# Kernel optimization log

Measured on AMD Instinct MI355X. Metric: run time of the kernel, lower is better.

Reference implementation:

```python
import jax, jax.numpy as jnp
import numpy as np

H = 16
D_MODEL = 1024
B, S = 2, 2048
DH = D_MODEL // H


def setup_inputs() -> dict:
    key = jax.random.key(0)
    ks = jax.random.split(key, 12)
    std = 0.02
    q = jax.random.normal(ks[0], (B, S, D_MODEL), dtype=jnp.float32)
    k = jax.random.normal(ks[1], (B, S, D_MODEL), dtype=jnp.float32)
    v = jax.random.normal(ks[2], (B, S, D_MODEL), dtype=jnp.float32)
    # additive causal mask: 0 on/below diagonal, -1e9 above
    causal = jnp.tril(jnp.ones((S, S), dtype=bool))
    mask = jnp.where(causal, 0.0, -1e9).astype(jnp.float32)[None, None, :, :]
    def dense(kk):
        return (jax.random.normal(kk, (D_MODEL, D_MODEL), dtype=jnp.float32) * std,
                jnp.zeros((D_MODEL,), dtype=jnp.float32))
    Wq, bq = dense(ks[3])
    Wk, bk = dense(ks[4])
    Wv, bv = dense(ks[5])
    Wo, bo = dense(ks[6])
    return {"q": q, "k": k, "v": v, "mask": mask,
            "Wq": Wq, "bq": bq, "Wk": Wk, "bk": bk,
            "Wv": Wv, "bv": bv, "Wo": Wo, "bo": bo}


def reference(q, k, v, mask, Wq, bq, Wk, bk, Wv, bv, Wo, bo):
    b, s, d = q.shape
    def split_heads(x):  # [b,s,d] -> [b,h,s,dh]
        return x.reshape(b, s, H, DH).transpose(0, 2, 1, 3)
    qh = split_heads(q @ Wq + bq)
    kh = split_heads(k @ Wk + bk)
    vh = split_heads(v @ Wv + bv)
    scale = 1.0 / jnp.sqrt(jnp.asarray(DH, dtype=qh.dtype))
    scores = jnp.einsum('bhqd,bhkd->bhqk', qh, kh) * scale + mask
    weights = jax.nn.softmax(scores, axis=-1)
    ctx = jnp.einsum('bhqk,bhkd->bhqd', weights, vh)
    ctx = ctx.transpose(0, 2, 1, 3).reshape(b, s, d)
    return ctx @ Wo + bo
```

## Files before the change

### kernel.cpp

```cpp
#include <hip/hip_runtime.h>
#include <hip/hip_bf16.h>
#include <stdint.h>

typedef __bf16 bf16x8 __attribute__((ext_vector_type(8)));
typedef float  f32x4  __attribute__((ext_vector_type(4)));
typedef __hip_bfloat16 bf16_t;

#define D_MODEL 1024
#define NH 16
#define DH 64
#define BB 2
#define SS 2048
#define MTOT (BB*SS)
#define NQT (SS/64)

#define GBM 128
#define GBN 64
#define GBK 64

__global__ void cvt_qkv_kernel(const float* __restrict__ q, const float* __restrict__ k,
                               const float* __restrict__ v, bf16_t* __restrict__ dst) {
  const int n1v = MTOT * D_MODEL / 4;
  int tid = blockIdx.x * blockDim.x + threadIdx.x;
  int stride = gridDim.x * blockDim.x;
  for (int i = tid; i < 3 * n1v; i += stride) {
    int which = i / n1v;
    int j = i - which * n1v;
    const float4* src = (const float4*)(which == 0 ? q : (which == 1 ? k : v));
    float4 f = src[j];
    union { bf16_t h[4]; short4 s4; } u;
    u.h[0] = __float2bfloat16(f.x);
    u.h[1] = __float2bfloat16(f.y);
    u.h[2] = __float2bfloat16(f.z);
    u.h[3] = __float2bfloat16(f.w);
    ((short4*)dst)[(size_t)which * n1v + j] = u.s4;
  }
}

__global__ void transpose_w_kernel(const float* __restrict__ W0, const float* __restrict__ W1,
                                   const float* __restrict__ W2, const float* __restrict__ W3,
                                   bf16_t* __restrict__ WtAll) {
  __shared__ float tile[32][33];
  const int z = blockIdx.z;
  const float* W = (z == 0) ? W0 : (z == 1) ? W1 : (z == 2) ? W2 : W3;
  bf16_t* Wt = WtAll + (size_t)z * D_MODEL * D_MODEL;
  const int tx = threadIdx.x, ty = threadIdx.y;
  const int bx = blockIdx.x, by = blockIdx.y;
#pragma unroll
  for (int i = 0; i < 4; ++i)
    tile[ty + i * 8][tx] = W[(size_t)(by * 32 + ty + i * 8) * D_MODEL + bx * 32 + tx];
  __syncthreads();
#pragma unroll
  for (int i = 0; i < 4; ++i)
    Wt[(size_t)(bx * 32 + ty + i * 8) * D_MODEL + by * 32 + tx] =
        __float2bfloat16(tile[tx][ty + i * 8]);
}

__device__ __forceinline__ void g2lds16(const bf16_t* g, bf16_t* l) {
  __builtin_amdgcn_global_load_lds((__attribute__((address_space(1))) void*)(g),
                                   (__attribute__((address_space(3))) void*)(l), 16, 0, 0);
}

__device__ __forceinline__ void gemm_tile_mainloop(const bf16_t* __restrict__ A,
                                                   const bf16_t* __restrict__ Bt,
                                                   bf16_t* As, bf16_t* Bs,
                                                   int m0, int n0, f32x4 acc[4][2]) {
  const int tid = threadIdx.x;
  const int wv = tid >> 6, ln = tid & 63;
  const int wr = wv >> 1, wc = wv & 1;
  const int lr = ln & 15, lg = ln >> 4;

#pragma unroll
  for (int mi = 0; mi < 4; ++mi)
#pragma unroll
    for (int ni = 0; ni < 2; ++ni)
      acc[mi][ni] = (f32x4){0.f, 0.f, 0.f, 0.f};

  for (int kt = 0; kt < D_MODEL / GBK; ++kt) {
#pragma unroll
    for (int c = 0; c < 6; ++c) {
      int chunk = wv * 6 + c;
      int row8 = ln >> 3;
      int col = (ln & 7) * 8;
      if (chunk < 16) {
        g2lds16(A  + (size_t)(m0 + chunk * 8 + row8) * D_MODEL + kt * GBK + col,
                As + chunk * 8 * GBK);
      } else {
        g2lds16(Bt + (size_t)(n0 + (chunk - 16) * 8 + row8) * D_MODEL + kt * GBK + col,
                Bs + (chunk - 16) * 8 * GBK);
      }
    }
    __syncthreads();
#pragma unroll
    for (int ks = 0; ks < 2; ++ks) {
      bf16x8 af[4], bfr[2];
#pragma unroll
      for (int mi = 0; mi < 4; ++mi)
        af[mi] = *(const bf16x8*)(As + (size_t)(wr * 64 + mi * 16 + lr) * GBK + ks * 32 + lg * 8);
#pragma unroll
      for (int ni = 0; ni < 2; ++ni)
        bfr[ni] = *(const bf16x8*)(Bs + (size_t)(wc * 32 + ni * 16 + lr) * GBK + ks * 32 + lg * 8);
#pragma unroll
      for (int mi = 0; mi < 4; ++mi)
#pragma unroll
        for (int ni = 0; ni < 2; ++ni)
          acc[mi][ni] = __builtin_amdgcn_mfma_f32_16x16x32_bf16(af[mi], bfr[ni], acc[mi][ni], 0, 0, 0);
    }
    __syncthreads();
  }
}

__global__ __launch_bounds__(256)
void proj_gemm_kernel(const bf16_t* __restrict__ Aq, const bf16_t* __restrict__ Ak,
                      const bf16_t* __restrict__ Av, const bf16_t* __restrict__ WtAll,
                      const float* __restrict__ bq, const float* __restrict__ bk,
                      const float* __restrict__ bv,
                      bf16_t* __restrict__ Qg, bf16_t* __restrict__ Kg,
                      bf16_t* __restrict__ Vt) {
  __shared__ bf16_t As[GBM * GBK];
  __shared__ bf16_t Bs[GBN * GBK];
  const int z = blockIdx.z;
  const bf16_t* A = (z == 0) ? Aq : (z == 1) ? Ak : Av;
  const bf16_t* Bt = WtAll + (size_t)z * D_MODEL * D_MODEL;
  const float* bias = (z == 0) ? bq : (z == 1) ? bk : bv;
  const int m0 = blockIdx.y * GBM, n0 = blockIdx.x * GBN;

  f32x4 acc[4][2];
  gemm_tile_mainloop(A, Bt, As, Bs, m0, n0, acc);

  const int tid = threadIdx.x;
  const int wv = tid >> 6, ln = tid & 63;
  const int wr = wv >> 1, wc = wv & 1;
  const int lr = ln & 15, lg = ln >> 4;

#pragma unroll
  for (int mi = 0; mi < 4; ++mi) {
#pragma unroll
    for (int ni = 0; ni < 2; ++ni) {
      int ncol = n0 + wc * 32 + ni * 16 + lr;
      float bsv = bias[ncol];
#pragma unroll
      for (int j = 0; j < 4; ++j) {
        int mrow = m0 + wr * 64 + mi * 16 + lg * 4 + j;
        bf16_t hv = __float2bfloat16(acc[mi][ni][j] + bsv);
        if (z == 0) {
          Qg[(size_t)mrow * D_MODEL + ncol] = hv;
        } else if (z == 1) {
          Kg[(size_t)mrow * D_MODEL + ncol] = hv;
        } else {
          int b = mrow >> 11, s = mrow & (SS - 1);
          Vt[(size_t)((b << 10) | ncol) * SS + s] = hv;
        }
      }
    }
  }
}

__global__ __launch_bounds__(256)
void out_gemm_kernel(const bf16_t* __restrict__ Ctx, const bf16_t* __restrict__ Wto,
                     const float* __restrict__ bo, float* __restrict__ out) {
  __shared__ bf16_t As[GBM * GBK];
  __shared__ bf16_t Bs[GBN * GBK];
  const int m0 = blockIdx.y * GBM, n0 = blockIdx.x * GBN;

  f32x4 acc[4][2];
  gemm_tile_mainloop(Ctx, Wto, As, Bs, m0, n0, acc);

  const int tid = threadIdx.x;
  const int wv = tid >> 6, ln = tid & 63;
  const int wr = wv >> 1, wc = wv & 1;
  const int lr = ln & 15, lg = ln >> 4;

#pragma unroll
  for (int mi = 0; mi < 4; ++mi) {
#pragma unroll
    for (int ni = 0; ni < 2; ++ni) {
      int ncol = n0 + wc * 32 + ni * 16 + lr;
      float bsv = bo[ncol];
#pragma unroll
      for (int j = 0; j < 4; ++j) {
        int mrow = m0 + wr * 64 + mi * 16 + lg * 4 + j;
        out[(size_t)mrow * D_MODEL + ncol] = acc[mi][ni][j] + bsv;
      }
    }
  }
}

__device__ __forceinline__ uint32_t pack2bf(float a, float b) {
  union { __hip_bfloat16 h; unsigned short u; } ua, ub;
  ua.h = __float2bfloat16(a);
  ub.h = __float2bfloat16(b);
  return (uint32_t)ua.u | ((uint32_t)ub.u << 16);
}

#define PSTRIDE 44

__device__ __forceinline__ void attn_run(
    f32x4 acc_o[2][4], f32x4 acc_l[2], float m_run[2],
    const bf16x8 qf[2][2], const bf16_t* Kbase, const bf16_t* Vbase,
    uint32_t (*P32)[PSTRIDE], int q0, int t0, int t1, int lr, int lg, bf16x8 onesf) {
  bf16x8 kf_cur[2][4];
#pragma unroll
  for (int ks = 0; ks < 2; ++ks)
#pragma unroll
    for (int kb = 0; kb < 4; ++kb)
      kf_cur[ks][kb] = *(const bf16x8*)(Kbase + (size_t)(t0 * 64 + kb * 16 + lr) * D_MODEL + ks * 32 + lg * 8);

  for (int t = t0; t < t1; ++t) {
    const int kv0 = t * 64;
    f32x4 sc[2][4];
#pragma unroll
    for (int qi = 0; qi < 2; ++qi)
#pragma unroll
      for (int kb = 0; kb < 4; ++kb) sc[qi][kb] = (f32x4){0.f, 0.f, 0.f, 0.f};

    __builtin_amdgcn_s_setprio(1);
#pragma unroll
    for (int ks = 0; ks < 2; ++ks) {
#pragma unroll
      for (int kb = 0; kb < 4; ++kb) {
        sc[0][kb] = __builtin_amdgcn_mfma_f32_16x16x32_bf16(kf_cur[ks][kb], qf[0][ks], sc[0][kb], 0, 0, 0);
        sc[1][kb] = __builtin_amdgcn_mfma_f32_16x16x32_bf16(kf_cur[ks][kb], qf[1][ks], sc[1][kb], 0, 0, 0);
      }
    }
    __builtin_amdgcn_s_setprio(0);

    bf16x8 kf_nxt[2][4];
    if (t + 1 < t1) {
#pragma unroll
      for (int ks = 0; ks < 2; ++ks)
#pragma unroll
        for (int kb = 0; kb < 4; ++kb)
          kf_nxt[ks][kb] = *(const bf16x8*)(Kbase + (size_t)(kv0 + 64 + kb * 16 + lr) * D_MODEL + ks * 32 + lg * 8);
    }
    bf16x8 vf[2][4];
#pragma unroll
    for (int ks = 0; ks < 2; ++ks)
#pragma unroll
      for (int db = 0; db < 4; ++db)
        vf[ks][db] = *(const bf16x8*)(Vbase + (size_t)(db * 16 + lr) * SS + kv0 + ks * 32 + lg * 8);

    if (kv0 + 63 > q0) {
#pragma unroll
      for (int qi = 0; qi < 2; ++qi) {
        int qc = q0 + qi * 16 + lr;
#pragma unroll
        for (int kb = 0; kb < 4; ++kb)
#pragma unroll
          for (int r = 0; r < 4; ++r) {
            int kc = kv0 + kb * 16 + 4 * lg + r;
            if (kc > qc) sc[qi][kb][r] = -1e30f;
          }
      }
    }

#pragma unroll
    for (int qi = 0; qi < 2; ++qi) {
      float vm = sc[qi][0][0];
#pragma unroll
      for (int kb = 0; kb < 4; ++kb)
#pragma unroll
        for (int r = 0; r < 4; ++r) vm = fmaxf(vm, sc[qi][kb][r]);
      vm = fmaxf(vm, __shfl_xor(vm, 16, 64));
      vm = fmaxf(vm, __shfl_xor(vm, 32, 64));
      float mo = m_run[qi];
      float mn = fmaxf(mo, vm);
      float scl = __expf(mo - mn);
      m_run[qi] = mn;
#pragma unroll
      for (int kb = 0; kb < 4; ++kb)
#pragma unroll
        for (int hh = 0; hh < 2; ++hh) {
          float p0 = __expf(sc[qi][kb][2 * hh]     - mn);
          float p1 = __expf(sc[qi][kb][2 * hh + 1] - mn);
          P32[qi * 16 + lr][8 * kb + 2 * lg + hh] = pack2bf(p0, p1);
        }
#pragma unroll
      for (int r = 0; r < 4; ++r) acc_l[qi][r] *= scl;
#pragma unroll
      for (int db = 0; db < 4; ++db)
#pragma unroll
        for (int r = 0; r < 4; ++r) acc_o[qi][db][r] *= scl;
    }

    asm volatile("s_waitcnt lgkmcnt(0)" ::: "memory");
    __builtin_amdgcn_sched_barrier(0);

    bf16x8 pb[2][2];
#pragma unroll
    for (int qi = 0; qi < 2; ++qi)
#pragma unroll
      for (int ks = 0; ks < 2; ++ks)
        pb[qi][ks] = *(const bf16x8*)&P32[qi * 16 + lr][16 * ks + 4 * lg];

    __builtin_amdgcn_s_setprio(1);
#pragma unroll
    for (int ks = 0; ks < 2; ++ks) {
#pragma unroll
      for (int qi = 0; qi < 2; ++qi) {
        acc_l[qi] = __builtin_amdgcn_mfma_f32_16x16x32_bf16(onesf, pb[qi][ks], acc_l[qi], 0, 0, 0);
#pragma unroll
        for (int db = 0; db < 4; ++db)
          acc_o[qi][db] = __builtin_amdgcn_mfma_f32_16x16x32_bf16(vf[ks][db], pb[qi][ks], acc_o[qi][db], 0, 0, 0);
      }
    }
    __builtin_amdgcn_s_setprio(0);

    if (t + 1 < t1) {
#pragma unroll
      for (int ks = 0; ks < 2; ++ks)
#pragma unroll
        for (int kb = 0; kb < 4; ++kb)
          kf_cur[ks][kb] = kf_nxt[ks][kb];
    }
  }
}

__device__ __forceinline__ void attn_load_q(bf16x8 qf[2][2], const bf16_t* Qbase,
                                            int q0, int lr, int lg) {
#pragma unroll
  for (int qi = 0; qi < 2; ++qi)
#pragma unroll
    for (int ks = 0; ks < 2; ++ks) {
      bf16x8 raw = *(const bf16x8*)(Qbase + (size_t)(q0 + qi * 16 + lr) * D_MODEL + ks * 32 + lg * 8);
#pragma unroll
      for (int j = 0; j < 8; ++j) raw[j] = (__bf16)((float)raw[j] * 0.125f);
      qf[qi][ks] = raw;
    }
}

__device__ __forceinline__ void attn_init(f32x4 acc_o[2][4], f32x4 acc_l[2], float m_run[2]) {
#pragma unroll
  for (int qi = 0; qi < 2; ++qi) {
#pragma unroll
    for (int db = 0; db < 4; ++db) acc_o[qi][db] = (f32x4){0.f, 0.f, 0.f, 0.f};
    acc_l[qi] = (f32x4){0.f, 0.f, 0.f, 0.f};
    m_run[qi] = -1e30f;
  }
}

__device__ __forceinline__ void store_ctx_tile(
    uint32_t (*P32)[PSTRIDE], const f32x4 acc_o[2][4], const f32x4 acc_l[2],
    bf16_t* __restrict__ Ctx, int b, int h, int q0, int ln, int lr, int lg) {
#pragma unroll
  for (int qi = 0; qi < 2; ++qi) {
    float rl = 1.0f / acc_l[qi][0];
#pragma unroll
    for (int db = 0; db < 4; ++db)
#pragma unroll
      for (int hh = 0; hh < 2; ++hh)
        P32[qi * 16 + lr][8 * db + 2 * lg + hh] =
            pack2bf(acc_o[qi][db][2 * hh] * rl, acc_o[qi][db][2 * hh + 1] * rl);
  }
  asm volatile("s_waitcnt lgkmcnt(0)" ::: "memory");
  __builtin_amdgcn_sched_barrier(0);
#pragma unroll
  for (int c = 0; c < 4; ++c) {
    int row = (ln >> 2) + 16 * (c >> 1);
    int dwc = (ln & 3) * 4 + 16 * (c & 1);
    bf16x8 v = *(const bf16x8*)&P32[row][dwc];
    *(bf16x8*)(Ctx + (size_t)(b * SS + q0 + row) * D_MODEL + h * DH + dwc * 2) = v;
  }
}

__global__ __launch_bounds__(256)
void attn_kernel(const bf16_t* __restrict__ Qg, const bf16_t* __restrict__ Kg,
                 const bf16_t* __restrict__ Vt, bf16_t* __restrict__ Ctx) {
  __shared__ __align__(16) uint32_t P32[4][32][PSTRIDE];
  __shared__ __align__(16) float O_part[2][32][68];
  __shared__ float ml_part[2][32][2];
  const int bh = blockIdx.x;
  const int pp = blockIdx.y;
  const int b = bh >> 4, h = bh & 15;
  const int wv = threadIdx.x >> 6, ln = threadIdx.x & 63;
  const int lr = ln & 15, lg = ln >> 4;

  const int qt_lo = pp, qt_hi = NQT - 1 - pp;
  const int h0 = 16 - pp;
  const int rh = wv & 1;

  const size_t qkbase = (size_t)b * SS * D_MODEL + (size_t)h * DH;
  const bf16_t* Qbase = Qg + qkbase;
  const bf16_t* Kbase = Kg + qkbase;
  const bf16_t* Vbase = Vt + (size_t)(bh * 64) * SS;

  bf16x8 onesf;
#pragma unroll
  for (int j = 0; j < 8; ++j) onesf[j] = (__bf16)1.0f;

  bf16x8 qf[2][2];
  f32x4 acc_o[2][4];
  f32x4 acc_l[2];
  float m_run[2];
  const int q0_hi = qt_hi * 64 + rh * 32;

  if (wv < 2) {
    const int q0_lo = qt_lo * 64 + rh * 32;
    attn_load_q(qf, Qbase, q0_lo, lr, lg);
    attn_init(acc_o, acc_l, m_run);
    attn_run(acc_o, acc_l, m_run, qf, Kbase, Vbase, P32[wv], q0_lo, 0, pp + 1, lr, lg, onesf);
    store_ctx_tile(P32[wv], acc_o, acc_l, Ctx, b, h, q0_lo, ln, lr, lg);

    attn_load_q(qf, Qbase, q0_hi, lr, lg);
    attn_init(acc_o, acc_l, m_run);
    attn_run(acc_o, acc_l, m_run, qf, Kbase, Vbase, P32[wv], q0_hi, 0, h0, lr, lg, onesf);
  } else {
    attn_load_q(qf, Qbase, q0_hi, lr, lg);
    attn_init(acc_o, acc_l, m_run);
    attn_run(acc_o, acc_l, m_run, qf, Kbase, Vbase, P32[wv], q0_hi, h0, NQT - pp, lr, lg, onesf);
    const int pidx = wv - 2;
#pragma unroll
    for (int qi = 0; qi < 2; ++qi) {
#pragma unroll
      for (int db = 0; db < 4; ++db)
        *(f32x4*)&O_part[pidx][qi * 16 + lr][16 * db + 4 * lg] = acc_o[qi][db];
      if (lg == 0) {
        ml_part[pidx][qi * 16 + lr][0] = m_run[qi];
        ml_part[pidx][qi * 16 + lr][1] = acc_l[qi][0];
      }
    }
  }

  __syncthreads();

  if (wv < 2) {
#pragma unroll
    for (int qi = 0; qi < 2; ++qi) {
      float m1 = m_run[qi];
      float m2 = ml_part[wv][qi * 16 + lr][0];
      float mn = fmaxf(m1, m2);
      float a1 = __expf(m1 - mn);
      float a2 = __expf(m2 - mn);
      float l = a1 * acc_l[qi][0] + a2 * ml_part[wv][qi * 16 + lr][1];
#pragma unroll
      for (int db = 0; db < 4; ++db) {
        f32x4 po = *(const f32x4*)&O_part[wv][qi * 16 + lr][16 * db + 4 * lg];
#pragma unroll
        for (int r = 0; r < 4; ++r)
          acc_o[qi][db][r] = a1 * acc_o[qi][db][r] + a2 * po[r];
      }
      acc_l[qi] = (f32x4){l, l, l, l};
    }
    store_ctx_tile(P32[wv], acc_o, acc_l, Ctx, b, h, q0_hi, ln, lr, lg);
  }
}

extern "C" void kernel_launch(void* const* d_in, const int* in_sizes, int n_in,
                              void* d_out, int out_size, void* d_ws, size_t ws_size,
                              hipStream_t stream) {
  const float* q  = (const float*)d_in[0];
  const float* k  = (const float*)d_in[1];
  const float* v  = (const float*)d_in[2];
  const float* bq = (const float*)d_in[5];
  const float* bk = (const float*)d_in[7];
  const float* bv = (const float*)d_in[9];
  const float* bo = (const float*)d_in[11];
  const float* Wq = (const float*)d_in[4];
  const float* Wk = (const float*)d_in[6];
  const float* Wv = (const float*)d_in[8];
  const float* Wo = (const float*)d_in[10];
  float* out = (float*)d_out;

  char* w = (char*)d_ws;
  bf16_t* Aqkv  = (bf16_t*)(w);
  bf16_t* WtAll = (bf16_t*)(w + 25165824);
  bf16_t* Qg    = (bf16_t*)(w + 33554432);
  bf16_t* Kg    = (bf16_t*)(w + 41943040);
  bf16_t* Vt    = (bf16_t*)(w + 50331648);
  bf16_t* Ctx   = (bf16_t*)(w + 58720256);

  cvt_qkv_kernel<<<2048, 256, 0, stream>>>(q, k, v, Aqkv);
  transpose_w_kernel<<<dim3(32, 32, 4), dim3(32, 8), 0, stream>>>(Wq, Wk, Wv, Wo, WtAll);
  proj_gemm_kernel<<<dim3(16, 32, 3), 256, 0, stream>>>(
      Aqkv, Aqkv + (size_t)MTOT * D_MODEL, Aqkv + 2 * (size_t)MTOT * D_MODEL,
      WtAll, bq, bk, bv, Qg, Kg, Vt);
  attn_kernel<<<dim3(32, 16), 256, 0, stream>>>(Qg, Kg, Vt, Ctx);
  out_gemm_kernel<<<dim3(16, 32), 256, 0, stream>>>(
      Ctx, WtAll + 3 * (size_t)D_MODEL * D_MODEL, bo, out);
}
```

Baseline: 275.6 us.

## Compute V-transpose projection directly as Wv^T·X^T and fold Q scale into projection

The V projection moves to its own kernel that computes Vt = Wv^T · Xv^T directly, by swapping the GEMM operands. Its stores are now coalesced along the sequence dimension instead of strided scatter writes, and Vt becomes a [1024, B*S] layout that attention indexes with stride MTOT. The 1/sqrt(dh) scale is applied in the Q projection epilogue, which removes the per-element rescale when attention loads Q. The cost is an extra kernel launch, and the V GEMM now runs as a separate, smaller grid.

```diff
diff --git a/kernel.cpp b/kernel.cpp
--- a/kernel.cpp
+++ b/kernel.cpp
@@ -111,18 +111,18 @@
 }
 
 __global__ __launch_bounds__(256)
-void proj_gemm_kernel(const bf16_t* __restrict__ Aq, const bf16_t* __restrict__ Ak,
-                      const bf16_t* __restrict__ Av, const bf16_t* __restrict__ WtAll,
-                      const float* __restrict__ bq, const float* __restrict__ bk,
-                      const float* __restrict__ bv,
-                      bf16_t* __restrict__ Qg, bf16_t* __restrict__ Kg,
-                      bf16_t* __restrict__ Vt) {
+void qk_proj_kernel(const bf16_t* __restrict__ Aq, const bf16_t* __restrict__ Ak,
+                    const bf16_t* __restrict__ WtAll,
+                    const float* __restrict__ bq, const float* __restrict__ bk,
+                    bf16_t* __restrict__ Qg, bf16_t* __restrict__ Kg) {
   __shared__ bf16_t As[GBM * GBK];
   __shared__ bf16_t Bs[GBN * GBK];
   const int z = blockIdx.z;
-  const bf16_t* A = (z == 0) ? Aq : (z == 1) ? Ak : Av;
+  const bf16_t* A = (z == 0) ? Aq : Ak;
   const bf16_t* Bt = WtAll + (size_t)z * D_MODEL * D_MODEL;
-  const float* bias = (z == 0) ? bq : (z == 1) ? bk : bv;
+  const float* bias = (z == 0) ? bq : bk;
+  bf16_t* Out = (z == 0) ? Qg : Kg;
+  const float scale = (z == 0) ? 0.125f : 1.0f;
   const int m0 = blockIdx.y * GBM, n0 = blockIdx.x * GBN;
 
   f32x4 acc[4][2];
@@ -142,15 +142,36 @@
 #pragma unroll
       for (int j = 0; j < 4; ++j) {
         int mrow = m0 + wr * 64 + mi * 16 + lg * 4 + j;
-        bf16_t hv = __float2bfloat16(acc[mi][ni][j] + bsv);
-        if (z == 0) {
-          Qg[(size_t)mrow * D_MODEL + ncol] = hv;
-        } else if (z == 1) {
-          Kg[(size_t)mrow * D_MODEL + ncol] = hv;
-        } else {
-          int b = mrow >> 11, s = mrow & (SS - 1);
-          Vt[(size_t)((b << 10) | ncol) * SS + s] = hv;
-        }
+        Out[(size_t)mrow * D_MODEL + ncol] = __float2bfloat16((acc[mi][ni][j] + bsv) * scale);
+      }
+    }
+  }
+}
+
+__global__ __launch_bounds__(256)
+void vt_proj_kernel(const bf16_t* __restrict__ Wtv, const bf16_t* __restrict__ Av,
+                    const float* __restrict__ bv, bf16_t* __restrict__ Vt) {
+  __shared__ bf16_t As[GBM * GBK];
+  __shared__ bf16_t Bs[GBN * GBK];
+  const int m0 = blockIdx.y * GBM, n0 = blockIdx.x * GBN;
+
+  f32x4 acc[4][2];
+  gemm_tile_mainloop(Wtv, Av, As, Bs, m0, n0, acc);
+
+  const int tid = threadIdx.x;
+  const int wv = tid >> 6, ln = tid & 63;
+  const int wr = wv >> 1, wc = wv & 1;
+  const int lr = ln & 15, lg = ln >> 4;
+
+#pragma unroll
+  for (int mi = 0; mi < 4; ++mi) {
+#pragma unroll
+    for (int ni = 0; ni < 2; ++ni) {
+      int ncol = n0 + wc * 32 + ni * 16 + lr;
+#pragma unroll
+      for (int j = 0; j < 4; ++j) {
+        int mrow = m0 + wr * 64 + mi * 16 + lg * 4 + j;
+        Vt[(size_t)mrow * MTOT + ncol] = __float2bfloat16(acc[mi][ni][j] + bv[mrow]);
       }
     }
   }
@@ -238,7 +259,7 @@
     for (int ks = 0; ks < 2; ++ks)
 #pragma unroll
       for (int db = 0; db < 4; ++db)
-        vf[ks][db] = *(const bf16x8*)(Vbase + (size_t)(db * 16 + lr) * SS + kv0 + ks * 32 + lg * 8);
+        vf[ks][db] = *(const bf16x8*)(Vbase + (size_t)(db * 16 + lr) * MTOT + kv0 + ks * 32 + lg * 8);
 
     if (kv0 + 63 > q0) {
 #pragma unroll
@@ -321,12 +342,8 @@
 #pragma unroll
   for (int qi = 0; qi < 2; ++qi)
 #pragma unroll
-    for (int ks = 0; ks < 2; ++ks) {
-      bf16x8 raw = *(const bf16x8*)(Qbase + (size_t)(q0 + qi * 16 + lr) * D_MODEL + ks * 32 + lg * 8);
-#pragma unroll
-      for (int j = 0; j < 8; ++j) raw[j] = (__bf16)((float)raw[j] * 0.125f);
-      qf[qi][ks] = raw;
-    }
+    for (int ks = 0; ks < 2; ++ks)
+      qf[qi][ks] = *(const bf16x8*)(Qbase + (size_t)(q0 + qi * 16 + lr) * D_MODEL + ks * 32 + lg * 8);
 }
 
 __device__ __forceinline__ void attn_init(f32x4 acc_o[2][4], f32x4 acc_l[2], float m_run[2]) {
@@ -382,7 +399,7 @@
   const size_t qkbase = (size_t)b * SS * D_MODEL + (size_t)h * DH;
   const bf16_t* Qbase = Qg + qkbase;
   const bf16_t* Kbase = Kg + qkbase;
-  const bf16_t* Vbase = Vt + (size_t)(bh * 64) * SS;
+  const bf16_t* Vbase = Vt + (size_t)(h * DH) * MTOT + b * SS;
 
   bf16x8 onesf;
 #pragma unroll
@@ -471,9 +488,10 @@
 
   cvt_qkv_kernel<<<2048, 256, 0, stream>>>(q, k, v, Aqkv);
   transpose_w_kernel<<<dim3(32, 32, 4), dim3(32, 8), 0, stream>>>(Wq, Wk, Wv, Wo, WtAll);
-  proj_gemm_kernel<<<dim3(16, 32, 3), 256, 0, stream>>>(
-      Aqkv, Aqkv + (size_t)MTOT * D_MODEL, Aqkv + 2 * (size_t)MTOT * D_MODEL,
-      WtAll, bq, bk, bv, Qg, Kg, Vt);
+  qk_proj_kernel<<<dim3(16, 32, 2), 256, 0, stream>>>(
+      Aqkv, Aqkv + (size_t)MTOT * D_MODEL, WtAll, bq, bk, Qg, Kg);
+  vt_proj_kernel<<<dim3(64, 8), 256, 0, stream>>>(
+      WtAll + 2 * (size_t)D_MODEL * D_MODEL, Aqkv + 2 * (size_t)MTOT * D_MODEL, bv, Vt);
   attn_kernel<<<dim3(32, 16), 256, 0, stream>>>(Qg, Kg, Vt, Ctx);
   out_gemm_kernel<<<dim3(16, 32), 256, 0, stream>>>(
       Ctx, WtAll + 3 * (size_t)D_MODEL * D_MODEL, bo, out);
```

Measured after the change: 280.7 us. No clear change (+1.8%).
